# Kernel tuning notes

Measured on AMD Instinct MI355X. Metric: run time of the kernel, lower is better.

Reference implementation:

```python
import jax, jax.numpy as jnp
import numpy as np

NUM_EXPERTS = 8
IN_FEATURES = 1024
OUT_FEATURES = 1024
TOTAL_TOKENS = 8192


def setup_inputs() -> dict:
    key = jax.random.key(0)
    k_x, k_w, k_b = jax.random.split(key, 3)
    inputs = jax.random.normal(k_x, (TOTAL_TOKENS, IN_FEATURES), dtype=jnp.float32)
    # lecun_normal-style scale for the per-expert kernels
    kernel = jax.random.normal(k_w, (NUM_EXPERTS, IN_FEATURES, OUT_FEATURES), dtype=jnp.float32) / np.sqrt(IN_FEATURES)
    bias = jax.random.normal(k_b, (NUM_EXPERTS, OUT_FEATURES), dtype=jnp.float32) * 0.01
    # ragged group sizes that sum exactly to TOTAL_TOKENS (tokens pre-sorted by expert)
    rng = np.random.default_rng(0)
    gs = rng.multinomial(TOTAL_TOKENS, [1.0 / NUM_EXPERTS] * NUM_EXPERTS)
    group_sizes = jnp.asarray(gs, dtype=jnp.int32)
    return {"inputs": inputs, "group_sizes": group_sizes, "kernel": kernel, "bias": bias}


def reference(inputs, group_sizes, kernel, bias):
    # inputs: [T, in], kernel: [E, in, out], bias: [E, out], group_sizes: [E]
    E = kernel.shape[0]
    T = inputs.shape[0]
    # per-token expert id (tokens are sorted/grouped by expert)
    expert_ids = jnp.repeat(jnp.arange(E, dtype=jnp.int32), group_sizes, total_repeat_length=T)  # [T]
    onehot = jax.nn.one_hot(expert_ids, E, dtype=inputs.dtype)  # [T, E]
    # grouped ragged matmul: y[t] = x[t] @ W[expert_ids[t]]
    xe = jnp.einsum("te,ti->eti", onehot, inputs)  # [E, T, in], zero outside each expert's group
    y = jnp.einsum("eti,eio->to", xe, kernel)  # [T, out]
    # ragged bias expansion: bias of the owning expert per token
    y = y + jnp.take(bias, expert_ids, axis=0)
    return y
```

## Files before the change

### kernel.cpp

```cpp
#include <hip/hip_runtime.h>
#include <hip/hip_bf16.h>

#define KDIM 1024
#define NDIM 1024
#define NEXP 8
#define TTOK 8192
#define NT (KDIM / 32)

typedef __bf16 bf16x8 __attribute__((ext_vector_type(8)));
typedef __bf16 bf16x4 __attribute__((ext_vector_type(4)));
typedef float  f32x4  __attribute__((ext_vector_type(4)));

__device__ __forceinline__ void gl2lds16(const void* g, void* l) {
  __builtin_amdgcn_global_load_lds(
      (const __attribute__((address_space(1))) void*)g,
      (__attribute__((address_space(3))) void*)l, 16, 0, 0);
}


__global__ __launch_bounds__(256) void prepass(
    const float* __restrict__ x, const float* __restrict__ W,
    __bf16* __restrict__ swA, __bf16* __restrict__ swB)
{
  __shared__ __align__(16) __bf16 Lt[64 * 72];
  const int t = threadIdx.x;
  if (blockIdx.x < 1024) {
#pragma unroll
    for (int p = 0; p < 4; ++p) {
      int s = blockIdx.x * 1024 + p * 256 + t;
      int lane = s & 63, kt = (s >> 6) & 31, panel = s >> 11;
      int row = panel * 16 + (lane & 15);
      int k0 = kt * 32 + ((lane >> 4) << 3);
      const float* xp = x + (size_t)row * KDIM + k0;
      float4 a = *(const float4*)xp;
      float4 b = *(const float4*)(xp + 4);
      bf16x8 v;
      v[0] = (__bf16)a.x; v[1] = (__bf16)a.y; v[2] = (__bf16)a.z; v[3] = (__bf16)a.w;
      v[4] = (__bf16)b.x; v[5] = (__bf16)b.y; v[6] = (__bf16)b.z; v[7] = (__bf16)b.w;
      *(bf16x8*)(swA + (size_t)s * 8) = v;
    }
  } else {
    int bid = blockIdx.x - 1024;
    int e = bid >> 8, r = bid & 255;
    int k0 = (r >> 4) * 64, n0 = (r & 15) * 64;
    const float* Wp = W + (size_t)e * KDIM * NDIM;
    int rr0 = t >> 4, c4 = t & 15;
#pragma unroll
    for (int p = 0; p < 4; ++p) {
      int kk = rr0 + p * 16;
      float4 v = *(const float4*)(Wp + (size_t)(k0 + kk) * NDIM + n0 + c4 * 4);
      Lt[(c4 * 4 + 0) * 72 + kk] = (__bf16)v.x;
      Lt[(c4 * 4 + 1) * 72 + kk] = (__bf16)v.y;
      Lt[(c4 * 4 + 2) * 72 + kk] = (__bf16)v.z;
      Lt[(c4 * 4 + 3) * 72 + kk] = (__bf16)v.w;
    }
    __syncthreads();
#pragma unroll
    for (int q = 0; q < 2; ++q) {
      int slot = q * 256 + t;
      int lane = slot & 63, grp = slot >> 6;
      int np = grp & 3, kt2 = grp >> 2;
      int nl = np * 16 + (lane & 15);
      int kl = kt2 * 32 + ((lane >> 4) << 3);
      bf16x8 v = *(const bf16x8*)(Lt + nl * 72 + kl);
      int panel = (n0 >> 4) + np;
      int ktg = (k0 >> 5) + kt2;
      size_t sg = (((size_t)e * 64 + panel) * 32 + ktg) * 64 + lane;
      *(bf16x8*)(swB + sg * 8) = v;
    }
  }
}

__global__ __launch_bounds__(256, 3) void moe_gemm_lds(
    const __bf16* __restrict__ swA, const __bf16* __restrict__ swB,
    const int* __restrict__ gs, const float* __restrict__ bias,
    float* __restrict__ out)
{
  __shared__ __align__(16) __bf16 buf[3][8192];

  const int b = blockIdx.x;
  const int xcd = b & 7, bi = b >> 3;
  int y = xcd * 9 + bi % 9;
  const int nt = bi / 9;

  int e = 0, tile0 = 0, lo = 0, hi = 0, found = 0, off = 0;
#pragma unroll
  for (int i = 0; i < NEXP; ++i) {
    int g = gs[i];
    int first = off >> 7;
    int cnt = (g > 0) ? (((off + g - 1) >> 7) - first + 1) : 0;
    if (!found) {
      if (y < cnt) {
        found = 1; e = i; tile0 = (first + y) << 7;
        lo = max(tile0, off); hi = min(tile0 + 128, off + g);
      } else y -= cnt;
    }
    off += g;
  }
  if (!found) return;
  const int n0 = nt * 128;

  const int t = threadIdx.x, lane = t & 63, wv = t >> 6;
  const int wm = wv & 1, wn = wv >> 1, lm = lane & 15, lg = lane >> 4;

  const __bf16* gA0 = swA + (size_t)((tile0 >> 4) + wv) * 16384 + lane * 8;
  const __bf16* gA1 = swA + (size_t)((tile0 >> 4) + 4 + wv) * 16384 + lane * 8;
  const __bf16* gB0 = swB + (size_t)(e * 64 + (n0 >> 4) + wv) * 16384 + lane * 8;
  const __bf16* gB1 = swB + (size_t)(e * 64 + (n0 >> 4) + 4 + wv) * 16384 + lane * 8;

  auto stage = [&](int kt, int sb) {
    __bf16* l = &buf[sb][0];
    const int ko = kt * 512;
    gl2lds16(gA0 + ko, l + (size_t)(0 * 256 + wv * 64) * 8);
    gl2lds16(gA1 + ko, l + (size_t)(1 * 256 + wv * 64) * 8);
    gl2lds16(gB0 + ko, l + (size_t)(2 * 256 + wv * 64) * 8);
    gl2lds16(gB1 + ko, l + (size_t)(3 * 256 + wv * 64) * 8);
  };

  f32x4 acc[4][4] = {};
  auto compute = [&](const __bf16* l) {
    bf16x8 aF[4], bF[4];
#pragma unroll
    for (int i = 0; i < 4; ++i)
      aF[i] = *(const bf16x8*)(l + (size_t)((wm * 4 + i) * 64 + lane) * 8);
#pragma unroll
    for (int j = 0; j < 4; ++j)
      bF[j] = *(const bf16x8*)(l + 4096 + (size_t)((wn * 4 + j) * 64 + lane) * 8);
#pragma unroll
    for (int i = 0; i < 4; ++i)
#pragma unroll
      for (int j = 0; j < 4; ++j)
        acc[i][j] = __builtin_amdgcn_mfma_f32_16x16x32_bf16(aF[i], bF[j], acc[i][j], 0, 0, 0);
  };

  stage(0, 0);
  stage(1, 1);
#pragma unroll 1
  for (int kt = 0; kt < NT - 1; ++kt) {
    asm volatile("s_waitcnt vmcnt(4)" ::: "memory");
    asm volatile("s_barrier" ::: "memory");
    if (kt + 2 < NT) stage(kt + 2, (kt + 2) % 3);
    __builtin_amdgcn_sched_barrier(0);
    compute(&buf[kt % 3][0]);
  }
  asm volatile("s_waitcnt vmcnt(0)" ::: "memory");
  asm volatile("s_barrier" ::: "memory");
  compute(&buf[(NT - 1) % 3][0]);

  float bj[4];
#pragma unroll
  for (int j = 0; j < 4; ++j) bj[j] = bias[e * NDIM + n0 + wn * 64 + j * 16 + lm];
#pragma unroll
  for (int i = 0; i < 4; ++i)
#pragma unroll
    for (int r = 0; r < 4; ++r) {
      int rabs = tile0 + wm * 64 + i * 16 + lg * 4 + r;
      if (rabs >= lo && rabs < hi) {
#pragma unroll
        for (int j = 0; j < 4; ++j)
          out[(size_t)rabs * NDIM + n0 + wn * 64 + j * 16 + lm] = acc[i][j][r] + bj[j];
      }
    }
}

#define LDA 40
__global__ __launch_bounds__(256) void moe_gemm_kernel(
    const float* __restrict__ x, const int* __restrict__ gs,
    const float* __restrict__ W, const float* __restrict__ bias,
    float* __restrict__ out)
{
  __shared__ __bf16 Al[128 * LDA];
  __shared__ __bf16 Bl[128 * LDA];
  const int e = blockIdx.z, mt = blockIdx.y, nt = blockIdx.x;
  int off = 0;
#pragma unroll
  for (int i = 0; i < NEXP; ++i) { int g = gs[i]; if (i < e) off += g; }
  const int ge = gs[e];
  const int m0 = mt * 128;
  if (m0 >= ge) return;
  const int rows = min(128, ge - m0);
  const int row0 = off + m0;
  const int n0 = nt * 128;
  const int t = threadIdx.x, lane = t & 63, wv = t >> 6;
  const int wm = wv & 1, wn = wv >> 1, lm = lane & 15, lg = lane >> 4;
  const int am = t >> 3, kq = t & 7, nb = t & 127, kh = t >> 7;
  float4 aReg[4]; float bReg[16];
  const float* Wp = W + (size_t)e * KDIM * NDIM + n0 + nb;
  auto load_tile = [&](int kt) {
#pragma unroll
    for (int p = 0; p < 4; ++p) {
      int r = am + 32 * p;
      if (r < rows) aReg[p] = *(const float4*)(x + (size_t)(row0 + r) * KDIM + kt * 32 + kq * 4);
      else aReg[p] = make_float4(0.f, 0.f, 0.f, 0.f);
    }
    const float* wp = Wp + (size_t)(kt * 32 + kh * 16) * NDIM;
#pragma unroll
    for (int j = 0; j < 16; ++j) bReg[j] = wp[(size_t)j * NDIM];
  };
  auto store_tile = [&]() {
#pragma unroll
    for (int p = 0; p < 4; ++p) {
      bf16x4 v;
      v[0] = (__bf16)aReg[p].x; v[1] = (__bf16)aReg[p].y;
      v[2] = (__bf16)aReg[p].z; v[3] = (__bf16)aReg[p].w;
      *(bf16x4*)(Al + (am + 32 * p) * LDA + kq * 4) = v;
    }
    bf16x8 b0, b1;
#pragma unroll
    for (int j = 0; j < 8; ++j) { b0[j] = (__bf16)bReg[j]; b1[j] = (__bf16)bReg[8 + j]; }
    *(bf16x8*)(Bl + nb * LDA + kh * 16) = b0;
    *(bf16x8*)(Bl + nb * LDA + kh * 16 + 8) = b1;
  };
  f32x4 acc[4][4] = {};
  load_tile(0);
#pragma unroll 1
  for (int kt = 0; kt < KDIM / 32; ++kt) {
    __syncthreads();
    store_tile();
    __syncthreads();
    if (kt + 1 < KDIM / 32) load_tile(kt + 1);
    bf16x8 af[4], bfr[4];
#pragma unroll
    for (int i = 0; i < 4; ++i)
      af[i] = *(const bf16x8*)(Al + (wm * 64 + i * 16 + lm) * LDA + lg * 8);
#pragma unroll
    for (int j = 0; j < 4; ++j)
      bfr[j] = *(const bf16x8*)(Bl + (wn * 64 + j * 16 + lm) * LDA + lg * 8);
#pragma unroll
    for (int i = 0; i < 4; ++i)
#pragma unroll
      for (int j = 0; j < 4; ++j)
        acc[i][j] = __builtin_amdgcn_mfma_f32_16x16x32_bf16(af[i], bfr[j], acc[i][j], 0, 0, 0);
  }
  float bj[4];
#pragma unroll
  for (int j = 0; j < 4; ++j) bj[j] = bias[e * NDIM + n0 + wn * 64 + j * 16 + lm];
#pragma unroll
  for (int i = 0; i < 4; ++i)
#pragma unroll
    for (int r = 0; r < 4; ++r) {
      int rr = wm * 64 + i * 16 + lg * 4 + r;
      if (rr < rows) {
#pragma unroll
        for (int j = 0; j < 4; ++j)
          out[(size_t)(row0 + rr) * NDIM + n0 + wn * 64 + j * 16 + lm] = acc[i][j][r] + bj[j];
      }
    }
}

extern "C" void kernel_launch(void* const* d_in, const int* in_sizes, int n_in,
                              void* d_out, int out_size, void* d_ws, size_t ws_size,
                              hipStream_t stream) {
  const float* x    = (const float*)d_in[0];
  const int*   gs   = (const int*)d_in[1];
  const float* W    = (const float*)d_in[2];
  const float* bias = (const float*)d_in[3];
  float*       out  = (float*)d_out;

  const size_t swA_bytes = (size_t)TTOK * KDIM * 2;
  const size_t swB_bytes = (size_t)NEXP * KDIM * NDIM * 2;
  if (ws_size >= swA_bytes + swB_bytes) {
    __bf16* swA = (__bf16*)d_ws;
    __bf16* swB = (__bf16*)((char*)d_ws + swA_bytes);
    prepass<<<dim3(1024 + 2048), 256, 0, stream>>>(x, W, swA, swB);
    moe_gemm_lds<<<dim3(576), 256, 0, stream>>>(swA, swB, gs, bias, out);
  } else {
    moe_gemm_kernel<<<dim3(NDIM / 128, TTOK / 128, NEXP), 256, 0, stream>>>(x, gs, W, bias, out);
  }
}
```

Baseline: 131.9 us.

## Fuse bf16 prepass and grouped GEMM into one cooperative kernel with grid sync

Merges the fp32-to-bf16 conversion/swizzle prepass and the grouped GEMM into a single cooperative kernel of 576 blocks. The blocks grid-stride over the prepass work, then hit a grid-wide barrier before running the GEMM tiles. The goal is to drop one kernel launch and the gap between launches. In exchange, the prepass runs on fewer resident blocks and a grid sync is added. If the cooperative launch fails, the code falls back to the original two-kernel path.

```diff
diff --git a/kernel.cpp b/kernel.cpp
--- a/kernel.cpp
+++ b/kernel.cpp
@@ -1,5 +1,8 @@
 #include <hip/hip_runtime.h>
 #include <hip/hip_bf16.h>
+#include <hip/hip_cooperative_groups.h>
+
+namespace cg = cooperative_groups;
 
 #define KDIM 1024
 #define NDIM 1024
@@ -17,6 +20,155 @@
       (__attribute__((address_space(3))) void*)l, 16, 0, 0);
 }
 
+
+__global__ __launch_bounds__(256, 3) void moe_fused(
+    const float* __restrict__ x, const float* __restrict__ W,
+    const int* __restrict__ gs, const float* __restrict__ bias,
+    __bf16* __restrict__ swA, __bf16* __restrict__ swB,
+    float* __restrict__ out)
+{
+  __shared__ __align__(16) __bf16 buf[3][8192];
+  const int t = threadIdx.x;
+
+  {
+    __bf16* Lt = &buf[0][0];
+    for (int vb = blockIdx.x; vb < 3072; vb += gridDim.x) {
+      if (vb < 1024) {
+#pragma unroll
+        for (int p = 0; p < 4; ++p) {
+          int s = vb * 1024 + p * 256 + t;
+          int lane = s & 63, kt = (s >> 6) & 31, panel = s >> 11;
+          int row = panel * 16 + (lane & 15);
+          int k0 = kt * 32 + ((lane >> 4) << 3);
+          const float* xp = x + (size_t)row * KDIM + k0;
+          float4 a = *(const float4*)xp;
+          float4 b = *(const float4*)(xp + 4);
+          bf16x8 v;
+          v[0] = (__bf16)a.x; v[1] = (__bf16)a.y; v[2] = (__bf16)a.z; v[3] = (__bf16)a.w;
+          v[4] = (__bf16)b.x; v[5] = (__bf16)b.y; v[6] = (__bf16)b.z; v[7] = (__bf16)b.w;
+          *(bf16x8*)(swA + (size_t)s * 8) = v;
+        }
+      } else {
+        int bid = vb - 1024;
+        int e = bid >> 8, r = bid & 255;
+        int k0 = (r >> 4) * 64, n0 = (r & 15) * 64;
+        const float* Wp = W + (size_t)e * KDIM * NDIM;
+        int rr0 = t >> 4, c4 = t & 15;
+        __syncthreads();
+#pragma unroll
+        for (int p = 0; p < 4; ++p) {
+          int kk = rr0 + p * 16;
+          float4 v = *(const float4*)(Wp + (size_t)(k0 + kk) * NDIM + n0 + c4 * 4);
+          Lt[(c4 * 4 + 0) * 72 + kk] = (__bf16)v.x;
+          Lt[(c4 * 4 + 1) * 72 + kk] = (__bf16)v.y;
+          Lt[(c4 * 4 + 2) * 72 + kk] = (__bf16)v.z;
+          Lt[(c4 * 4 + 3) * 72 + kk] = (__bf16)v.w;
+        }
+        __syncthreads();
+#pragma unroll
+        for (int q = 0; q < 2; ++q) {
+          int slot = q * 256 + t;
+          int lane = slot & 63, grp = slot >> 6;
+          int np = grp & 3, kt2 = grp >> 2;
+          int nl = np * 16 + (lane & 15);
+          int kl = kt2 * 32 + ((lane >> 4) << 3);
+          bf16x8 v = *(const bf16x8*)(Lt + nl * 72 + kl);
+          int panel = (n0 >> 4) + np;
+          int ktg = (k0 >> 5) + kt2;
+          size_t sg = (((size_t)e * 64 + panel) * 32 + ktg) * 64 + lane;
+          *(bf16x8*)(swB + sg * 8) = v;
+        }
+      }
+    }
+  }
+
+  __threadfence();
+  cg::this_grid().sync();
+
+  const int b = blockIdx.x;
+  const int xcd = b & 7, bi = b >> 3;
+  int y = xcd * 9 + bi % 9;
+  const int nt = bi / 9;
+
+  int e = 0, tile0 = 0, lo = 0, hi = 0, found = 0, off = 0;
+#pragma unroll
+  for (int i = 0; i < NEXP; ++i) {
+    int g = gs[i];
+    int first = off >> 7;
+    int cnt = (g > 0) ? (((off + g - 1) >> 7) - first + 1) : 0;
+    if (!found) {
+      if (y < cnt) {
+        found = 1; e = i; tile0 = (first + y) << 7;
+        lo = max(tile0, off); hi = min(tile0 + 128, off + g);
+      } else y -= cnt;
+    }
+    off += g;
+  }
+  if (!found) return;
+  const int n0 = nt * 128;
+
+  const int lane = t & 63, wv = t >> 6;
+  const int wm = wv & 1, wn = wv >> 1, lm = lane & 15, lg = lane >> 4;
+
+  const __bf16* gA0 = swA + (size_t)((tile0 >> 4) + wv) * 16384 + lane * 8;
+  const __bf16* gA1 = swA + (size_t)((tile0 >> 4) + 4 + wv) * 16384 + lane * 8;
+  const __bf16* gB0 = swB + (size_t)(e * 64 + (n0 >> 4) + wv) * 16384 + lane * 8;
+  const __bf16* gB1 = swB + (size_t)(e * 64 + (n0 >> 4) + 4 + wv) * 16384 + lane * 8;
+
+  auto stage = [&](int kt, int sb) {
+    __bf16* l = &buf[sb][0];
+    const int ko = kt * 512;
+    gl2lds16(gA0 + ko, l + (size_t)(0 * 256 + wv * 64) * 8);
+    gl2lds16(gA1 + ko, l + (size_t)(1 * 256 + wv * 64) * 8);
+    gl2lds16(gB0 + ko, l + (size_t)(2 * 256 + wv * 64) * 8);
+    gl2lds16(gB1 + ko, l + (size_t)(3 * 256 + wv * 64) * 8);
+  };
+
+  f32x4 acc[4][4] = {};
+  auto compute = [&](const __bf16* l) {
+    bf16x8 aF[4], bF[4];
+#pragma unroll
+    for (int i = 0; i < 4; ++i)
+      aF[i] = *(const bf16x8*)(l + (size_t)((wm * 4 + i) * 64 + lane) * 8);
+#pragma unroll
+    for (int j = 0; j < 4; ++j)
+      bF[j] = *(const bf16x8*)(l + 4096 + (size_t)((wn * 4 + j) * 64 + lane) * 8);
+#pragma unroll
+    for (int i = 0; i < 4; ++i)
+#pragma unroll
+      for (int j = 0; j < 4; ++j)
+        acc[i][j] = __builtin_amdgcn_mfma_f32_16x16x32_bf16(aF[i], bF[j], acc[i][j], 0, 0, 0);
+  };
+
+  stage(0, 0);
+  stage(1, 1);
+#pragma unroll 1
+  for (int kt = 0; kt < NT - 1; ++kt) {
+    asm volatile("s_waitcnt vmcnt(4)" ::: "memory");
+    asm volatile("s_barrier" ::: "memory");
+    if (kt + 2 < NT) stage(kt + 2, (kt + 2) % 3);
+    __builtin_amdgcn_sched_barrier(0);
+    compute(&buf[kt % 3][0]);
+  }
+  asm volatile("s_waitcnt vmcnt(0)" ::: "memory");
+  asm volatile("s_barrier" ::: "memory");
+  compute(&buf[(NT - 1) % 3][0]);
+
+  float bj[4];
+#pragma unroll
+  for (int j = 0; j < 4; ++j) bj[j] = bias[e * NDIM + n0 + wn * 64 + j * 16 + lm];
+#pragma unroll
+  for (int i = 0; i < 4; ++i)
+#pragma unroll
+    for (int r = 0; r < 4; ++r) {
+      int rabs = tile0 + wm * 64 + i * 16 + lg * 4 + r;
+      if (rabs >= lo && rabs < hi) {
+#pragma unroll
+        for (int j = 0; j < 4; ++j)
+          out[(size_t)rabs * NDIM + n0 + wn * 64 + j * 16 + lm] = acc[i][j][r] + bj[j];
+      }
+    }
+}
 
 __global__ __launch_bounds__(256) void prepass(
     const float* __restrict__ x, const float* __restrict__ W,
@@ -262,8 +414,14 @@
   if (ws_size >= swA_bytes + swB_bytes) {
     __bf16* swA = (__bf16*)d_ws;
     __bf16* swB = (__bf16*)((char*)d_ws + swA_bytes);
-    prepass<<<dim3(1024 + 2048), 256, 0, stream>>>(x, W, swA, swB);
-    moe_gemm_lds<<<dim3(576), 256, 0, stream>>>(swA, swB, gs, bias, out);
+    void* args[] = {(void*)&x, (void*)&W, (void*)&gs, (void*)&bias,
+                    (void*)&swA, (void*)&swB, (void*)&out};
+    hipError_t err = hipLaunchCooperativeKernel(
+        (const void*)moe_fused, dim3(576), dim3(256), args, 0, stream);
+    if (err != hipSuccess) {
+      prepass<<<dim3(1024 + 2048), 256, 0, stream>>>(x, W, swA, swB);
+      moe_gemm_lds<<<dim3(576), 256, 0, stream>>>(swA, swB, gs, bias, out);
+    }
   } else {
     moe_gemm_kernel<<<dim3(NDIM / 128, TTOK / 128, NEXP), 256, 0, stream>>>(x, gs, W, bias, out);
   }
```

Result: slower. 290.8 us (+120.6%).
